# Optimization experiments

Measured on AMD Instinct MI355X. Metric: run time of the kernel, lower is better.

The kernel has to match this reference:

```python
import jax, jax.numpy as jnp
import numpy as np

N, K, D = 1000000, 4, 16

def setup_inputs() -> dict:
    key = jax.random.key(0)
    k1, k2, k3, k4, k5 = jax.random.split(key, 5)
    z = jax.random.normal(k1, (N, D), dtype=jnp.float32)
    phi = jax.nn.softmax(jax.random.normal(k2, (K,), dtype=jnp.float32))  # mixture weights, sum to 1
    mu = jax.random.normal(k3, (K, D), dtype=jnp.float32)
    # Upper-triangular Cholesky-like factor with positive diagonal (module calls
    # solve_triangular(..., upper=True), i.e. L is treated as upper triangular).
    A = jax.random.normal(k4, (K, D, D), dtype=jnp.float32) * 0.1
    diag = 0.8 + 0.4 * jax.random.uniform(k5, (K, D), dtype=jnp.float32)
    L = jnp.triu(A, 1) + jnp.zeros((K, D, D), jnp.float32).at[:, jnp.arange(D), jnp.arange(D)].set(diag)
    return {"z": z, "phi": phi, "mu": mu, "L": L}

def reference(z, phi, mu, L):
    # z: [N,D], phi: [K], mu: [K,D], L: [K,D,D] upper-triangular
    z_centered = z[:, None, :] - mu[None, :, :]            # [N,K,D]
    b = jnp.transpose(z_centered, (1, 2, 0))               # [K,D,N]
    v = jax.lax.linalg.triangular_solve(L, b, left_side=True, lower=False)  # [K,D,N]
    log_det_sigma = 2.0 * jnp.sum(jnp.log(jnp.diagonal(L, axis1=-2, axis2=-1)), axis=1)  # [K]
    d = z.shape[1]
    logits = jnp.log(phi)[:, None] - 0.5 * (
        jnp.sum(jnp.square(v), axis=1)                     # [K,N] Mahalanobis term
        + d * jnp.log(2.0 * jnp.pi)
        + log_det_sigma[:, None]
    )                                                      # [K,N]
    energies = -jax.scipy.special.logsumexp(logits, axis=0)  # [N]
    return energies
```

## Files before the change

### kernel.cpp

```cpp
#include <hip/hip_runtime.h>
#include <math.h>

namespace {

constexpr int KK = 4;
constexpr int DD = 16;
constexpr int BLOCK = 256;
constexpr int PTS = 2;
constexpr float LOG2PI = 1.8378770664093453f;
constexpr float INV_SQRT2 = 0.70710678118654752f;

constexpr int WOFF_W  = KK * DD * DD;
constexpr int WOFF_C0 = WOFF_W + KK * DD;

__global__ void gmm_prep(const float* __restrict__ phi, const float* __restrict__ mu,
                         const float* __restrict__ L, float* __restrict__ ws)
{
    const int tid = threadIdx.x;
    const int k = tid >> 4;
    const int j = tid & 15;
    const float* __restrict__ Lk = L + k * DD * DD;

    float xv[DD];
    #pragma unroll
    for (int m = 0; m < DD; ++m) xv[m] = 0.0f;
    #pragma unroll
    for (int i = DD - 1; i >= 0; --i) {
        float s = (i == j) ? 1.0f : 0.0f;
        #pragma unroll
        for (int m = i + 1; m < DD; ++m)
            s = fmaf(-Lk[i * DD + m], xv[m], s);
        xv[i] = (i <= j) ? (s / Lk[i * DD + i]) : 0.0f;
    }
    #pragma unroll
    for (int i = 0; i < DD; ++i)
        ws[k * DD * DD + i * DD + j] = xv[i] * INV_SQRT2;

    __syncthreads();

    float w = 0.0f;
    #pragma unroll
    for (int jj = 0; jj < DD; ++jj)
        w = fmaf(ws[k * DD * DD + j * DD + jj], mu[k * DD + jj], w);
    ws[WOFF_W + k * DD + j] = w;

    if (tid < KK) {
        float logdet = 0.0f;
        #pragma unroll
        for (int i = 0; i < DD; ++i)
            logdet += __logf(L[tid * DD * DD + i * DD + i]);
        ws[WOFF_C0 + tid] = __logf(phi[tid]) - 8.0f * LOG2PI - logdet;
    }
}

__global__ __launch_bounds__(BLOCK, 4)
void gmm_energy(const float* __restrict__ z, const float* __restrict__ cw,
                float* __restrict__ out, int N)
{
    const int tid = threadIdx.x;
    const int base = blockIdx.x * (BLOCK * PTS) + tid * PTS;
    const bool full = (base + PTS <= N);

    float zr[PTS][DD];
    if (full) {
        #pragma unroll
        for (int p = 0; p < PTS; ++p) {
            const float4* zp = reinterpret_cast<const float4*>(z + (size_t)(base + p) * DD);
            #pragma unroll
            for (int c = 0; c < 4; ++c) {
                float4 v = zp[c];
                zr[p][c * 4 + 0] = v.x;
                zr[p][c * 4 + 1] = v.y;
                zr[p][c * 4 + 2] = v.z;
                zr[p][c * 4 + 3] = v.w;
            }
        }
    } else {
        #pragma unroll
        for (int p = 0; p < PTS; ++p) {
            if (base + p < N) {
                const float4* zp = reinterpret_cast<const float4*>(z + (size_t)(base + p) * DD);
                #pragma unroll
                for (int c = 0; c < 4; ++c) {
                    float4 v = zp[c];
                    zr[p][c * 4 + 0] = v.x;
                    zr[p][c * 4 + 1] = v.y;
                    zr[p][c * 4 + 2] = v.z;
                    zr[p][c * 4 + 3] = v.w;
                }
            } else {
                #pragma unroll
                for (int d = 0; d < DD; ++d) zr[p][d] = 0.0f;
            }
        }
    }

    float lg[PTS][KK];
    #pragma unroll
    for (int k = 0; k < KK; ++k) {
        const float* __restrict__ Ck = cw + k * DD * DD;
        const float* __restrict__ Wk = cw + WOFF_W + k * DD;
        float q[PTS];
        #pragma unroll
        for (int p = 0; p < PTS; ++p) q[p] = 0.0f;
        #pragma unroll
        for (int i = 0; i < DD; ++i) {
            const float wk = Wk[i];
            float acc[PTS];
            #pragma unroll
            for (int p = 0; p < PTS; ++p)
                acc[p] = fmaf(Ck[i * DD + i], zr[p][i], -wk);
            #pragma unroll
            for (int j = i + 1; j < DD; ++j) {
                const float cf = Ck[i * DD + j];
                #pragma unroll
                for (int p = 0; p < PTS; ++p)
                    acc[p] = fmaf(cf, zr[p][j], acc[p]);
            }
            #pragma unroll
            for (int p = 0; p < PTS; ++p)
                q[p] = fmaf(acc[p], acc[p], q[p]);
        }
        const float c0 = cw[WOFF_C0 + k];
        #pragma unroll
        for (int p = 0; p < PTS; ++p)
            lg[p][k] = c0 - q[p];
    }

    float e[PTS];
    #pragma unroll
    for (int p = 0; p < PTS; ++p) {
        float m01 = fmaxf(lg[p][0], lg[p][1]);
        float m23 = fmaxf(lg[p][2], lg[p][3]);
        float m = fmaxf(m01, m23);
        float s = __expf(lg[p][0] - m) + __expf(lg[p][1] - m)
                + __expf(lg[p][2] - m) + __expf(lg[p][3] - m);
        e[p] = -(m + __logf(s));
    }

    if (full) {
        float2 res;
        res.x = e[0]; res.y = e[1];
        *reinterpret_cast<float2*>(out + base) = res;
    } else {
        #pragma unroll
        for (int p = 0; p < PTS; ++p) {
            if (base + p < N) out[base + p] = e[p];
        }
    }
}

}

extern "C" void kernel_launch(void* const* d_in, const int* in_sizes, int n_in,
                              void* d_out, int out_size, void* d_ws, size_t ws_size,
                              hipStream_t stream) {
    const float* z   = (const float*)d_in[0];
    const float* phi = (const float*)d_in[1];
    const float* mu  = (const float*)d_in[2];
    const float* L   = (const float*)d_in[3];
    float* out = (float*)d_out;
    float* ws  = (float*)d_ws;
    const int N = in_sizes[0] / DD;

    gmm_prep<<<1, 64, 0, stream>>>(phi, mu, L, ws);

    const int grid = (N + BLOCK * PTS - 1) / (BLOCK * PTS);
    gmm_energy<<<grid, BLOCK, 0, stream>>>(z, ws, out, N);
}
```

Measured before the change: 113.7 us.

## Stage z tiles through swizzled shared memory for fully coalesced global loads

Full blocks now load their 512 points of z with fully coalesced float4 loads into a swizzled LDS buffer, then each thread reads its own two rows back from LDS. Before, each thread read its own 128 contiguous bytes, so a wave's accesses were strided. The register arrays are also rearranged to a dimension-major layout with explicit scalar accumulators. This costs 32KB of LDS per block and a barrier, which may limit occupancy.

```diff
diff --git a/kernel.cpp b/kernel.cpp
--- a/kernel.cpp
+++ b/kernel.cpp
@@ -7,6 +7,7 @@
 constexpr int DD = 16;
 constexpr int BLOCK = 256;
 constexpr int PTS = 2;
+constexpr int PBLK = BLOCK * PTS;
 constexpr float LOG2PI = 1.8378770664093453f;
 constexpr float INV_SQRT2 = 0.70710678118654752f;
 
@@ -55,24 +56,36 @@
 
 __global__ __launch_bounds__(BLOCK, 4)
 void gmm_energy(const float* __restrict__ z, const float* __restrict__ cw,
-                float* __restrict__ out, int N)
+                float* __restrict__ out, int N, int full_blocks)
 {
+    __shared__ float4 sz[PBLK * 4];
     const int tid = threadIdx.x;
-    const int base = blockIdx.x * (BLOCK * PTS) + tid * PTS;
-    const bool full = (base + PTS <= N);
+    const int base = blockIdx.x * PBLK + tid * PTS;
 
-    float zr[PTS][DD];
-    if (full) {
+    float zr[DD][PTS];
+
+    if (blockIdx.x < full_blocks) {
+        const float4* __restrict__ zsrc =
+            reinterpret_cast<const float4*>(z) + (size_t)blockIdx.x * (PBLK * 4);
+        #pragma unroll
+        for (int s = 0; s < 8; ++s) {
+            const int lin = s * BLOCK + tid;
+            const int swz = (lin & ~7) | ((lin ^ (lin >> 3)) & 7);
+            sz[swz] = zsrc[lin];
+        }
+        __syncthreads();
         #pragma unroll
         for (int p = 0; p < PTS; ++p) {
-            const float4* zp = reinterpret_cast<const float4*>(z + (size_t)(base + p) * DD);
+            const int r = tid * PTS + p;
+            const int rev = r >> 1;
             #pragma unroll
             for (int c = 0; c < 4; ++c) {
-                float4 v = zp[c];
-                zr[p][c * 4 + 0] = v.x;
-                zr[p][c * 4 + 1] = v.y;
-                zr[p][c * 4 + 2] = v.z;
-                zr[p][c * 4 + 3] = v.w;
+                const int slot = (((r & 1) << 2) | c) ^ (rev & 7);
+                const float4 v = sz[rev * 8 + slot];
+                zr[c * 4 + 0][p] = v.x;
+                zr[c * 4 + 1][p] = v.y;
+                zr[c * 4 + 2][p] = v.z;
+                zr[c * 4 + 3][p] = v.w;
             }
         }
     } else {
@@ -82,63 +95,57 @@
                 const float4* zp = reinterpret_cast<const float4*>(z + (size_t)(base + p) * DD);
                 #pragma unroll
                 for (int c = 0; c < 4; ++c) {
-                    float4 v = zp[c];
-                    zr[p][c * 4 + 0] = v.x;
-                    zr[p][c * 4 + 1] = v.y;
-                    zr[p][c * 4 + 2] = v.z;
-                    zr[p][c * 4 + 3] = v.w;
+                    const float4 v = zp[c];
+                    zr[c * 4 + 0][p] = v.x;
+                    zr[c * 4 + 1][p] = v.y;
+                    zr[c * 4 + 2][p] = v.z;
+                    zr[c * 4 + 3][p] = v.w;
                 }
             } else {
                 #pragma unroll
-                for (int d = 0; d < DD; ++d) zr[p][d] = 0.0f;
+                for (int d = 0; d < DD; ++d) zr[d][p] = 0.0f;
             }
         }
     }
 
-    float lg[PTS][KK];
+    float lg[KK][PTS];
     #pragma unroll
     for (int k = 0; k < KK; ++k) {
         const float* __restrict__ Ck = cw + k * DD * DD;
         const float* __restrict__ Wk = cw + WOFF_W + k * DD;
-        float q[PTS];
-        #pragma unroll
-        for (int p = 0; p < PTS; ++p) q[p] = 0.0f;
+        float q0 = 0.0f, q1 = 0.0f;
         #pragma unroll
         for (int i = 0; i < DD; ++i) {
             const float wk = Wk[i];
-            float acc[PTS];
-            #pragma unroll
-            for (int p = 0; p < PTS; ++p)
-                acc[p] = fmaf(Ck[i * DD + i], zr[p][i], -wk);
+            const float cd = Ck[i * DD + i];
+            float a0 = fmaf(cd, zr[i][0], -wk);
+            float a1 = fmaf(cd, zr[i][1], -wk);
             #pragma unroll
             for (int j = i + 1; j < DD; ++j) {
                 const float cf = Ck[i * DD + j];
-                #pragma unroll
-                for (int p = 0; p < PTS; ++p)
-                    acc[p] = fmaf(cf, zr[p][j], acc[p]);
+                a0 = fmaf(cf, zr[j][0], a0);
+                a1 = fmaf(cf, zr[j][1], a1);
             }
-            #pragma unroll
-            for (int p = 0; p < PTS; ++p)
-                q[p] = fmaf(acc[p], acc[p], q[p]);
+            q0 = fmaf(a0, a0, q0);
+            q1 = fmaf(a1, a1, q1);
         }
         const float c0 = cw[WOFF_C0 + k];
-        #pragma unroll
-        for (int p = 0; p < PTS; ++p)
-            lg[p][k] = c0 - q[p];
+        lg[k][0] = c0 - q0;
+        lg[k][1] = c0 - q1;
     }
 
     float e[PTS];
     #pragma unroll
     for (int p = 0; p < PTS; ++p) {
-        float m01 = fmaxf(lg[p][0], lg[p][1]);
-        float m23 = fmaxf(lg[p][2], lg[p][3]);
+        float m01 = fmaxf(lg[0][p], lg[1][p]);
+        float m23 = fmaxf(lg[2][p], lg[3][p]);
         float m = fmaxf(m01, m23);
-        float s = __expf(lg[p][0] - m) + __expf(lg[p][1] - m)
-                + __expf(lg[p][2] - m) + __expf(lg[p][3] - m);
+        float s = __expf(lg[0][p] - m) + __expf(lg[1][p] - m)
+                + __expf(lg[2][p] - m) + __expf(lg[3][p] - m);
         e[p] = -(m + __logf(s));
     }
 
-    if (full) {
+    if (base + PTS <= N) {
         float2 res;
         res.x = e[0]; res.y = e[1];
         *reinterpret_cast<float2*>(out + base) = res;
@@ -165,6 +172,7 @@
 
     gmm_prep<<<1, 64, 0, stream>>>(phi, mu, L, ws);
 
-    const int grid = (N + BLOCK * PTS - 1) / (BLOCK * PTS);
-    gmm_energy<<<grid, BLOCK, 0, stream>>>(z, ws, out, N);
+    const int full_blocks = N / PBLK;
+    const int grid = (N + PBLK - 1) / PBLK;
+    gmm_energy<<<grid, BLOCK, 0, stream>>>(z, ws, out, N, full_blocks);
 }
```

New measurement: 118.4 us. 1.04x slower.
